# Optimization experiments

Hardware: AMD Instinct MI355X
Metric: run time of the kernel (lower is better)

## Reference

```python
import jax, jax.numpy as jnp
import numpy as np

N_NODES = 50000
N_EDGES = 800000
IN_C = 16
HID_C = 16
OUT_C = 10
N_GRAPHS = 500
EDGE_DIM = 3
MLP_HID = 25
BN_EPS = 1e-5


def setup_inputs() -> dict:
    key = jax.random.key(0)
    ks = iter(jax.random.split(key, 40))

    def nrm(shape, scale=1.0):
        return jax.random.normal(next(ks), shape, dtype=jnp.float32) * scale

    inp = {}
    inp["x"] = nrm((N_NODES, IN_C))
    inp["edge_index"] = jax.random.randint(next(ks), (2, N_EDGES), 0, N_NODES, dtype=jnp.int32)
    inp["edge_attr"] = jax.random.uniform(next(ks), (N_EDGES, EDGE_DIM), dtype=jnp.float32)
    inp["batch"] = jnp.sort(jax.random.randint(next(ks), (N_NODES,), 0, N_GRAPHS, dtype=jnp.int32))

    def bn_params():
        g = jax.random.uniform(next(ks), (MLP_HID,), minval=0.8, maxval=1.2, dtype=jnp.float32)
        b = nrm((MLP_HID,), 0.1)
        mu = nrm((MLP_HID,), 0.1)
        var = jax.random.uniform(next(ks), (MLP_HID,), minval=0.5, maxval=1.5, dtype=jnp.float32)
        return g, b, mu, var

    # edge MLP 1: 3 -> 25 -> IN_C*HID_C
    inp["W1a"] = nrm((EDGE_DIM, MLP_HID), 0.3)
    inp["b1a"] = nrm((MLP_HID,), 0.05)
    inp["g1"], inp["bt1"], inp["m1"], inp["v1"] = bn_params()
    inp["W1b"] = nrm((MLP_HID, IN_C * HID_C), 0.1)
    inp["b1b"] = nrm((IN_C * HID_C,), 0.05)
    inp["root1"] = nrm((IN_C, HID_C), 0.2)
    inp["bias1"] = nrm((HID_C,), 0.05)

    # edge MLP 2: 3 -> 25 -> HID_C*HID_C
    inp["W2a"] = nrm((EDGE_DIM, MLP_HID), 0.3)
    inp["b2a"] = nrm((MLP_HID,), 0.05)
    inp["g2"], inp["bt2"], inp["m2"], inp["v2"] = bn_params()
    inp["W2b"] = nrm((MLP_HID, HID_C * HID_C), 0.1)
    inp["b2b"] = nrm((HID_C * HID_C,), 0.05)
    inp["root2"] = nrm((HID_C, HID_C), 0.2)
    inp["bias2"] = nrm((HID_C,), 0.05)

    # final MLP([HID_C, OUT_C]) -> single plain linear (plain_last)
    inp["fcW"] = nrm((HID_C, OUT_C), 0.2)
    inp["fcb"] = nrm((OUT_C,), 0.05)
    return inp


def _edge_mlp(e, Wa, ba, g, bt, mu, var, Wb, bb):
    # Linear -> BatchNorm(eval) -> ReLU -> (dropout=eval identity) -> Linear
    h = e @ Wa + ba
    h = g * (h - mu) * jax.lax.rsqrt(var + BN_EPS) + bt
    h = jax.nn.relu(h)
    return h @ Wb + bb


def _nnconv(x, src, dst, w_edge, root, bias, out_dim):
    # message: x_j [E,in] times per-edge weight [E,in,out]
    msg = jnp.einsum("ei,eio->eo", x[src], w_edge)
    agg = jax.ops.segment_sum(msg, dst, num_segments=N_NODES)
    deg = jax.ops.segment_sum(jnp.ones((src.shape[0],), msg.dtype), dst, num_segments=N_NODES)
    agg = agg / jnp.maximum(deg, 1.0)[:, None]  # mean aggregation
    return agg + x @ root + bias


def reference(x, edge_index, edge_attr, batch,
              W1a, b1a, g1, bt1, m1, v1, W1b, b1b, root1, bias1,
              W2a, b2a, g2, bt2, m2, v2, W2b, b2b, root2, bias2,
              fcW, fcb):
    src, dst = edge_index[0], edge_index[1]

    w1 = _edge_mlp(edge_attr, W1a, b1a, g1, bt1, m1, v1, W1b, b1b).reshape(-1, IN_C, HID_C)
    x = jax.nn.elu(_nnconv(x, src, dst, w1, root1, bias1, HID_C))

    w2 = _edge_mlp(edge_attr, W2a, b2a, g2, bt2, m2, v2, W2b, b2b).reshape(-1, HID_C, HID_C)
    x = jax.nn.elu(_nnconv(x, src, dst, w2, root2, bias2, HID_C))

    # global mean pooling over graphs
    pooled = jax.ops.segment_sum(x, batch, num_segments=N_GRAPHS)
    cnt = jax.ops.segment_sum(jnp.ones((x.shape[0],), x.dtype), batch, num_segments=N_GRAPHS)
    pooled = pooled / jnp.maximum(cnt, 1.0)[:, None]

    return pooled @ fcW + fcb  # [N_GRAPHS, OUT_C]
```

## Files before the change

kernel.cpp:

```cpp
#include <hip/hip_runtime.h>
#include <math.h>

#define N_NODES 50000
#define N_EDGES 800000
#define IN_C 16
#define HID_C 16
#define OUT_C 10
#define N_GRAPHS 500
#define EDGE_DIM 3
#define MLP_HID 25
#define BN_EPS 1e-5f

#define SCAN_NB ((N_NODES + 255) / 256)

typedef __attribute__((ext_vector_type(8))) _Float16 half8;
typedef __attribute__((ext_vector_type(2))) _Float16 half2v;
typedef __attribute__((ext_vector_type(4))) float f32x4;
union U4H8 { uint4 u; half8 h; half2v p[4]; };
union HU { _Float16 h; unsigned short u; };
union H2U2 { half2v p[2]; uint2 u; };


__global__ __launch_bounds__(256) void setup_kernel(
    const float* __restrict__ W1a, const float* __restrict__ b1a,
    const float* __restrict__ g1, const float* __restrict__ bt1,
    const float* __restrict__ m1, const float* __restrict__ v1,
    const float* __restrict__ W2a, const float* __restrict__ b2a,
    const float* __restrict__ g2, const float* __restrict__ bt2,
    const float* __restrict__ m2, const float* __restrict__ v2,
    const float* __restrict__ W1b, const float* __restrict__ b1b,
    const float* __restrict__ W2b, const float* __restrict__ b2b,
    const int* __restrict__ batch,
    float* __restrict__ AC1, float* __restrict__ AC2,
    unsigned int* __restrict__ WF1, unsigned int* __restrict__ WF2,
    int* __restrict__ goff, int* __restrict__ cnt, int* __restrict__ flag)
{
    const int blk = blockIdx.x;
    const int tid = threadIdx.x;
    if (blk < 7) {
        int t = blk * 256 + tid;
        if (t >= 1664) return;
        const float *Wb, *bb; unsigned int *WH;
        int tl = t;
        if (t < 832) { Wb = W1b; bb = b1b; WH = WF1; }
        else { tl = t - 832; Wb = W2b; bb = b2b; WH = WF2; }
        int m = tl >> 6;
        int L = tl & 63;
        int q = L >> 4, o = L & 15;
        unsigned int hi[8];
        for (int j = 0; j < 8; ++j) {
            int kp = m*32 + q*8 + j;
            int k = kp >> 4, i = kp & 15;
            float w = (k < 25) ? Wb[k*256 + i*16 + o] : bb[i*16 + o];
            HU cv; cv.h = (_Float16)w;
            hi[j] = cv.u;
        }
        int base = (m*64 + L) * 4;
        for (int d = 0; d < 4; ++d)
            WH[base + d] = hi[2*d] | (hi[2*d+1] << 16);
        return;
    }
    if (blk == 7 || blk == 8) {
        if (blk == 7) {
            if (tid < 26) {
                int k = tid;
                if (k < 25) {
                    float sc = g1[k] / sqrtf(v1[k] + BN_EPS);
                    AC1[k*4+0] = sc * W1a[0*MLP_HID+k];
                    AC1[k*4+1] = sc * W1a[1*MLP_HID+k];
                    AC1[k*4+2] = sc * W1a[2*MLP_HID+k];
                    AC1[k*4+3] = sc * (b1a[k] - m1[k]) + bt1[k];
                } else {
                    AC1[100] = 0.f; AC1[101] = 0.f; AC1[102] = 0.f; AC1[103] = 1.f;
                }
            } else if (tid >= 32 && tid < 58) {
                int k = tid - 32;
                if (k < 25) {
                    float sc = g2[k] / sqrtf(v2[k] + BN_EPS);
                    AC2[k*4+0] = sc * W2a[0*MLP_HID+k];
                    AC2[k*4+1] = sc * W2a[1*MLP_HID+k];
                    AC2[k*4+2] = sc * W2a[2*MLP_HID+k];
                    AC2[k*4+3] = sc * (b2a[k] - m2[k]) + bt2[k];
                } else {
                    AC2[100] = 0.f; AC2[101] = 0.f; AC2[102] = 0.f; AC2[103] = 1.f;
                }
            }
        }
        int g = (blk - 7) * 256 + tid;
        if (g <= N_GRAPHS) {
            int lo = 0, hi = N_NODES;
            while (lo < hi) {
                int mid = (lo + hi) >> 1;
                if (batch[mid] < g) lo = mid + 1; else hi = mid;
            }
            goff[g] = lo;
        }
        return;
    }
    int idx = (blk - 9) * 256 + tid;
    if (idx < N_NODES) cnt[idx] = 0;
    if (blk == 9 && tid < SCAN_NB) flag[tid] = 0;
}


__global__ __launch_bounds__(256) void rank_kernel(const int* __restrict__ dst,
                                                   int* __restrict__ cnt,
                                                   int* __restrict__ rank) {
    int e = blockIdx.x * blockDim.x + threadIdx.x;
    if (e < N_EDGES) rank[e] = atomicAdd(&cnt[dst[e]], 1);
}

__global__ __launch_bounds__(256) void scan_single(const int* __restrict__ cnt,
                                                   int* __restrict__ off,
                                                   int* __restrict__ agg,
                                                   int* __restrict__ pre,
                                                   int* __restrict__ flag) {
    __shared__ int lds[256];
    __shared__ int sExc;
    const int b = blockIdx.x, t = threadIdx.x;
    const int idx = b * 256 + t;
    const int v = (idx < N_NODES) ? cnt[idx] : 0;
    lds[t] = v;
    __syncthreads();
    for (int d = 1; d < 256; d <<= 1) {
        int u = (t >= d) ? lds[t - d] : 0;
        __syncthreads();
        lds[t] += u;
        __syncthreads();
    }
    const int total = lds[255];
    if (t == 0) {
        int exc = 0;
        if (b == 0) {
            atomicExch(&pre[0], total);
            __threadfence();
            atomicExch(&flag[0], 2);
        } else {
            atomicExch(&agg[b], total);
            __threadfence();
            atomicExch(&flag[b], 1);
            int j = b - 1;
            while (true) {
                int f;
                do { f = atomicAdd(&flag[j], 0); } while (f == 0);
                if (f == 2) { exc += atomicAdd(&pre[j], 0); break; }
                exc += atomicAdd(&agg[j], 0);
                --j;
            }
            atomicExch(&pre[b], exc + total);
            __threadfence();
            atomicExch(&flag[b], 2);
        }
        sExc = exc;
    }
    __syncthreads();
    const int exc = sExc;
    if (idx < N_NODES) off[idx] = exc + lds[t] - v;
    if (b == SCAN_NB - 1 && t == 255) off[N_NODES] = exc + total;
}


__global__ __launch_bounds__(256) void edge_mfma6_kernel(
    const float* __restrict__ xin,
    const int* __restrict__ src,
    const int* __restrict__ dst,
    const int* __restrict__ rank,
    const int* __restrict__ off,
    const float* __restrict__ eattr,
    const float* __restrict__ AC,
    const unsigned int* __restrict__ WF,
    _Float16* __restrict__ msg_buf)
{
    __shared__ uint4 wf_s[832];
    const int tid = threadIdx.x;
    #pragma unroll
    for (int it = 0; it < 4; ++it) {
        int gi = tid + it*256;
        if (gi < 832) wf_s[gi] = ((const uint4*)WF)[gi];
    }
    __syncthreads();

    const int wave = tid >> 6;
    const int lane = tid & 63;
    const int q    = lane >> 4;
    const int el   = lane & 15;
    const int i0   = (q & 1) * 8;
    const bool bsel = (q >> 1) != 0;
    const int E0   = (blockIdx.x * 4 + wave) * 64;

    const int sAll = src[E0 + lane];
    const int dAll = dst[E0 + lane];
    const int rAll = rank[E0 + lane];
    const int pAll = off[dAll] + rAll;

    int   sT[4];
    float a0[4], a1[4], a2[4];
    #pragma unroll
    for (int t = 0; t < 4; ++t) {
        sT[t] = __shfl(sAll, t*16 + el);
        int e = E0 + t*16 + el;
        a0[t] = eattr[(size_t)e*3+0];
        a1[t] = eattr[(size_t)e*3+1];
        a2[t] = eattr[(size_t)e*3+2];
    }

    U4H8 xf[4];
    #pragma unroll
    for (int t = 0; t < 4; ++t) {
        const float4* xp = (const float4*)(xin + (size_t)sT[t]*16 + i0);
        const float4 xl = xp[0], xh = xp[1];
        const float x8[8] = {xl.x,xl.y,xl.z,xl.w,xh.x,xh.y,xh.z,xh.w};
        #pragma unroll
        for (int j = 0; j < 4; ++j) {
            half2v tv; tv.x = (_Float16)x8[2*j]; tv.y = (_Float16)x8[2*j+1];
            xf[t].p[j] = tv;
        }
    }

    f32x4 acc0 = {0.f,0.f,0.f,0.f}, acc1 = {0.f,0.f,0.f,0.f};
    f32x4 acc2 = {0.f,0.f,0.f,0.f}, acc3 = {0.f,0.f,0.f,0.f};
    #pragma unroll 1
    for (int m = 0; m < 13; ++m) {
        const float4 Ae = *(const float4*)(AC + m*8);
        const float4 Ao = *(const float4*)(AC + m*8 + 4);
        const float A0 = bsel ? Ao.x : Ae.x;
        const float A1 = bsel ? Ao.y : Ae.y;
        const float A2 = bsel ? Ao.z : Ae.z;
        const float A3 = bsel ? Ao.w : Ae.w;
        U4H8 w; w.u = wf_s[m*64 + lane];
        #pragma unroll
        for (int t = 0; t < 4; ++t) {
            float h = fmaxf(fmaf(a2[t], A2, fmaf(a1[t], A1,
                              fmaf(a0[t], A0, A3))), 0.f);
            _Float16 hh = (_Float16)h;
            half2v h2; h2.x = hh; h2.y = hh;
            U4H8 f;
            #pragma unroll
            for (int j = 0; j < 4; ++j) f.p[j] = h2 * xf[t].p[j];
            f32x4 a = (t==0) ? acc0 : (t==1) ? acc1 : (t==2) ? acc2 : acc3;
            a = __builtin_amdgcn_mfma_f32_16x16x32_f16(w.h, f.h, a, 0, 0, 0);
            if (t==0) acc0 = a; else if (t==1) acc1 = a;
            else if (t==2) acc2 = a; else acc3 = a;
        }
    }

    #pragma unroll
    for (int t = 0; t < 4; ++t) {
        int row = __shfl(pAll, t*16 + el);
        f32x4 a = (t==0) ? acc0 : (t==1) ? acc1 : (t==2) ? acc2 : acc3;
        H2U2 cv;
        half2v c01; c01.x = (_Float16)a[0]; c01.y = (_Float16)a[1];
        half2v c23; c23.x = (_Float16)a[2]; c23.y = (_Float16)a[3];
        cv.p[0] = c01; cv.p[1] = c23;
        *(uint2*)(msg_buf + (size_t)row * HID_C + q*4) = cv.u;
    }
}

__global__ __launch_bounds__(256) void node_gather_kernel(
    const float* __restrict__ xin, const _Float16* __restrict__ msg_buf,
    const int* __restrict__ off,
    const float* __restrict__ root, const float* __restrict__ bias,
    float* __restrict__ xout)
{
    int t = blockIdx.x * blockDim.x + threadIdx.x;
    int n = t >> 2;
    int quad = t & 3;
    if (n >= N_NODES) return;
    int lo = off[n], hi = off[n+1];
    float inv = 1.f / fmaxf((float)(hi - lo), 1.f);

    f32x4 s0 = {0.f,0.f,0.f,0.f}, s1 = {0.f,0.f,0.f,0.f};
    int r = lo;
    for (; r + 2 <= hi; r += 2) {
        H2U2 c0; c0.u = *(const uint2*)(msg_buf + (size_t)r     * HID_C + quad*4);
        H2U2 c1; c1.u = *(const uint2*)(msg_buf + (size_t)(r+1) * HID_C + quad*4);
        s0[0] += (float)c0.p[0].x; s0[1] += (float)c0.p[0].y;
        s0[2] += (float)c0.p[1].x; s0[3] += (float)c0.p[1].y;
        s1[0] += (float)c1.p[0].x; s1[1] += (float)c1.p[0].y;
        s1[2] += (float)c1.p[1].x; s1[3] += (float)c1.p[1].y;
    }
    if (r < hi) {
        H2U2 c0; c0.u = *(const uint2*)(msg_buf + (size_t)r * HID_C + quad*4);
        s0[0] += (float)c0.p[0].x; s0[1] += (float)c0.p[0].y;
        s0[2] += (float)c0.p[1].x; s0[3] += (float)c0.p[1].y;
    }

    const float4 bi = *(const float4*)(bias + quad*4);
    float acc0 = fmaf(s0[0] + s1[0], inv, bi.x);
    float acc1 = fmaf(s0[1] + s1[1], inv, bi.y);
    float acc2 = fmaf(s0[2] + s1[2], inv, bi.z);
    float acc3 = fmaf(s0[3] + s1[3], inv, bi.w);

    const float4* xp = (const float4*)(xin + (size_t)n * IN_C);
    const float4 x0 = xp[0], x1 = xp[1], x2 = xp[2], x3 = xp[3];
    const float xr[16] = {x0.x,x0.y,x0.z,x0.w, x1.x,x1.y,x1.z,x1.w,
                          x2.x,x2.y,x2.z,x2.w, x3.x,x3.y,x3.z,x3.w};
    #pragma unroll
    for (int i = 0; i < IN_C; ++i) {
        const float4 rr = *(const float4*)(root + i*HID_C + quad*4);
        acc0 = fmaf(xr[i], rr.x, acc0);
        acc1 = fmaf(xr[i], rr.y, acc1);
        acc2 = fmaf(xr[i], rr.z, acc2);
        acc3 = fmaf(xr[i], rr.w, acc3);
    }
    float4 ov;
    ov.x = acc0 > 0.f ? acc0 : (expf(acc0) - 1.f);
    ov.y = acc1 > 0.f ? acc1 : (expf(acc1) - 1.f);
    ov.z = acc2 > 0.f ? acc2 : (expf(acc2) - 1.f);
    ov.w = acc3 > 0.f ? acc3 : (expf(acc3) - 1.f);
    *(float4*)(xout + (size_t)n*HID_C + quad*4) = ov;
}

__global__ __launch_bounds__(64) void pool_final_kernel(
    const float* __restrict__ xin, const int* __restrict__ goff,
    const float* __restrict__ fcW, const float* __restrict__ fcb,
    float* __restrict__ out)
{
    __shared__ float part[4][HID_C];
    __shared__ float pooled[HID_C];
    int g = blockIdx.x;
    int t = threadIdx.x;
    int c = t & 15, sub = t >> 4;
    int lo = goff[g], hi = goff[g+1];
    float s = 0.f;
    for (int n = lo + sub; n < hi; n += 4)
        s += xin[(size_t)n*HID_C + c];
    part[sub][c] = s;
    __syncthreads();
    if (t < HID_C) {
        pooled[t] = (part[0][t] + part[1][t] + part[2][t] + part[3][t])
                    / fmaxf((float)(hi - lo), 1.f);
    }
    __syncthreads();
    if (t < OUT_C) {
        float acc = fcb[t];
        #pragma unroll
        for (int i = 0; i < HID_C; ++i)
            acc = fmaf(pooled[i], fcW[i*OUT_C+t], acc);
        out[g*OUT_C + t] = acc;
    }
}


extern "C" void kernel_launch(void* const* d_in, const int* in_sizes, int n_in,
                              void* d_out, int out_size, void* d_ws, size_t ws_size,
                              hipStream_t stream)
{
    const float* x     = (const float*)d_in[0];
    const int*   ei    = (const int*)d_in[1];
    const float* eattr = (const float*)d_in[2];
    const int*   batch = (const int*)d_in[3];
    const float* W1a   = (const float*)d_in[4];
    const float* b1a   = (const float*)d_in[5];
    const float* g1    = (const float*)d_in[6];
    const float* bt1   = (const float*)d_in[7];
    const float* m1    = (const float*)d_in[8];
    const float* v1    = (const float*)d_in[9];
    const float* W1b   = (const float*)d_in[10];
    const float* b1b   = (const float*)d_in[11];
    const float* root1 = (const float*)d_in[12];
    const float* bias1 = (const float*)d_in[13];
    const float* W2a   = (const float*)d_in[14];
    const float* b2a   = (const float*)d_in[15];
    const float* g2    = (const float*)d_in[16];
    const float* bt2   = (const float*)d_in[17];
    const float* m2    = (const float*)d_in[18];
    const float* v2    = (const float*)d_in[19];
    const float* W2b   = (const float*)d_in[20];
    const float* b2b   = (const float*)d_in[21];
    const float* root2 = (const float*)d_in[22];
    const float* bias2 = (const float*)d_in[23];
    const float* fcW   = (const float*)d_in[24];
    const float* fcb   = (const float*)d_in[25];

    const int* src = ei;
    const int* dst = ei + N_EDGES;

    float* ws   = (float*)d_ws;
    _Float16* MSG = (_Float16*)ws;
    float* X1   = ws + 12800000;
    float* X2   = ws + 13600000;
    int*   RANK = (int*)(ws + 14400000);
    int*   CNT  = (int*)(ws + 15200000);
    int*   OFF  = (int*)(ws + 15250000);
    int*   GOFF = (int*)(ws + 15300064);
    unsigned int* WF1 = (unsigned int*)(ws + 15300576);
    unsigned int* WF2 = (unsigned int*)(ws + 15303904);
    float* AC1  = ws + 15307232;
    float* AC2  = ws + 15307344;
    int*   AGG  = (int*)(ws + 15307456);
    int*   PRE  = (int*)(ws + 15307712);
    int*   FLAG = (int*)(ws + 15307968);

    setup_kernel<<<9 + SCAN_NB, 256, 0, stream>>>(
        W1a, b1a, g1, bt1, m1, v1, W2a, b2a, g2, bt2, m2, v2,
        W1b, b1b, W2b, b2b, batch, AC1, AC2, WF1, WF2, GOFF, CNT, FLAG);
    rank_kernel<<<N_EDGES/256, 256, 0, stream>>>(dst, CNT, RANK);
    scan_single<<<SCAN_NB, 256, 0, stream>>>(CNT, OFF, AGG, PRE, FLAG);

    edge_mfma6_kernel<<<N_EDGES/256, 256, 0, stream>>>(x, src, dst, RANK, OFF,
                                                       eattr, AC1, WF1, MSG);
    node_gather_kernel<<<(N_NODES*4+255)/256, 256, 0, stream>>>(x, MSG, OFF,
                                                                root1, bias1, X1);

    edge_mfma6_kernel<<<N_EDGES/256, 256, 0, stream>>>(X1, src, dst, RANK, OFF,
                                                       eattr, AC2, WF2, MSG);
    node_gather_kernel<<<(N_NODES*4+255)/256, 256, 0, stream>>>(X1, MSG, OFF,
                                                                root2, bias2, X2);

    pool_final_kernel<<<N_GRAPHS, 64, 0, stream>>>(X2, GOFF, fcW, fcb, (float*)d_out);
}
```

Before: 261.4 us.

## Fuse all stages into a persistent megakernel with software grid barriers

Replaces the eight separate launches (setup, rank, scan, two edge MFMA passes, two gathers, pooling) with one persistent kernel of 1024 blocks. Stages are separated by an atomic generation-counter grid barrier, and the edge and rank phases use grid-stride loops. The aim is to remove per-launch overhead and the idle tails between dependent kernels. In exchange it adds seven global barrier round-trips, relies on all 1024 blocks being co-resident, and caps registers through launch bounds, which could reduce edge-phase occupancy or deadlock if the blocks do not all fit.

```diff
diff --git a/kernel.cpp b/kernel.cpp
--- a/kernel.cpp
+++ b/kernel.cpp
@@ -11,6 +11,8 @@
 #define MLP_HID 25
 #define BN_EPS 1e-5f
 
+#define NB_GRID 1024
+#define N_CHUNKS (N_EDGES / 256)
 #define SCAN_NB ((N_NODES + 255) / 256)
 
 typedef __attribute__((ext_vector_type(8))) _Float16 half8;
@@ -20,47 +22,228 @@
 union HU { _Float16 h; unsigned short u; };
 union H2U2 { half2v p[2]; uint2 u; };
 
-
-__global__ __launch_bounds__(256) void setup_kernel(
+__device__ __forceinline__ void grid_sync(int* bar, int* gen) {
+    __syncthreads();
+    if (threadIdx.x == 0) {
+        __threadfence();
+        int g = atomicAdd(gen, 0);
+        if (atomicAdd(bar, 1) == NB_GRID - 1) {
+            atomicExch(bar, 0);
+            __threadfence();
+            atomicAdd(gen, 1);
+        } else {
+            while (atomicAdd(gen, 0) == g) __builtin_amdgcn_s_sleep(8);
+        }
+        __threadfence();
+    }
+    __syncthreads();
+}
+
+__device__ __forceinline__ void edge_phase(
+    const float* __restrict__ xin, const int* __restrict__ src,
+    const int* __restrict__ dst, const int* __restrict__ rank,
+    const int* __restrict__ off, const float* __restrict__ eattr,
+    const float* __restrict__ AC, const uint4* __restrict__ WF,
+    _Float16* __restrict__ msg_buf, uint4* wf_s)
+{
+    const int tid = threadIdx.x;
+    #pragma unroll
+    for (int it = 0; it < 4; ++it) {
+        int gi = tid + it*256;
+        if (gi < 832) wf_s[gi] = WF[gi];
+    }
+    __syncthreads();
+
+    const int wave = tid >> 6;
+    const int lane = tid & 63;
+    const int q    = lane >> 4;
+    const int el   = lane & 15;
+    const int i0   = (q & 1) * 8;
+    const bool bsel = (q >> 1) != 0;
+
+    for (int chunk = blockIdx.x; chunk < N_CHUNKS; chunk += NB_GRID) {
+        const int E0 = (chunk * 4 + wave) * 64;
+
+        const int sAll = src[E0 + lane];
+        const int dAll = dst[E0 + lane];
+        const int rAll = rank[E0 + lane];
+        const int pAll = off[dAll] + rAll;
+
+        int   sT[4];
+        float a0[4], a1[4], a2[4];
+        #pragma unroll
+        for (int t = 0; t < 4; ++t) {
+            sT[t] = __shfl(sAll, t*16 + el);
+            int e = E0 + t*16 + el;
+            a0[t] = eattr[(size_t)e*3+0];
+            a1[t] = eattr[(size_t)e*3+1];
+            a2[t] = eattr[(size_t)e*3+2];
+        }
+
+        U4H8 xf[4];
+        #pragma unroll
+        for (int t = 0; t < 4; ++t) {
+            const float4* xp = (const float4*)(xin + (size_t)sT[t]*16 + i0);
+            const float4 xl = xp[0], xh = xp[1];
+            const float x8[8] = {xl.x,xl.y,xl.z,xl.w,xh.x,xh.y,xh.z,xh.w};
+            #pragma unroll
+            for (int j = 0; j < 4; ++j) {
+                half2v tv; tv.x = (_Float16)x8[2*j]; tv.y = (_Float16)x8[2*j+1];
+                xf[t].p[j] = tv;
+            }
+        }
+
+        f32x4 acc0 = {0.f,0.f,0.f,0.f}, acc1 = {0.f,0.f,0.f,0.f};
+        f32x4 acc2 = {0.f,0.f,0.f,0.f}, acc3 = {0.f,0.f,0.f,0.f};
+        #pragma unroll 1
+        for (int m = 0; m < 13; ++m) {
+            const float4 Ae = *(const float4*)(AC + m*8);
+            const float4 Ao = *(const float4*)(AC + m*8 + 4);
+            const float A0 = bsel ? Ao.x : Ae.x;
+            const float A1 = bsel ? Ao.y : Ae.y;
+            const float A2 = bsel ? Ao.z : Ae.z;
+            const float A3 = bsel ? Ao.w : Ae.w;
+            U4H8 w; w.u = wf_s[m*64 + lane];
+            #pragma unroll
+            for (int t = 0; t < 4; ++t) {
+                float h = fmaxf(fmaf(a2[t], A2, fmaf(a1[t], A1,
+                                  fmaf(a0[t], A0, A3))), 0.f);
+                _Float16 hh = (_Float16)h;
+                half2v h2; h2.x = hh; h2.y = hh;
+                U4H8 f;
+                #pragma unroll
+                for (int j = 0; j < 4; ++j) f.p[j] = h2 * xf[t].p[j];
+                f32x4 a = (t==0) ? acc0 : (t==1) ? acc1 : (t==2) ? acc2 : acc3;
+                a = __builtin_amdgcn_mfma_f32_16x16x32_f16(w.h, f.h, a, 0, 0, 0);
+                if (t==0) acc0 = a; else if (t==1) acc1 = a;
+                else if (t==2) acc2 = a; else acc3 = a;
+            }
+        }
+
+        #pragma unroll
+        for (int t = 0; t < 4; ++t) {
+            int row = __shfl(pAll, t*16 + el);
+            f32x4 a = (t==0) ? acc0 : (t==1) ? acc1 : (t==2) ? acc2 : acc3;
+            H2U2 cv;
+            half2v c01; c01.x = (_Float16)a[0]; c01.y = (_Float16)a[1];
+            half2v c23; c23.x = (_Float16)a[2]; c23.y = (_Float16)a[3];
+            cv.p[0] = c01; cv.p[1] = c23;
+            *(uint2*)(msg_buf + (size_t)row * HID_C + q*4) = cv.u;
+        }
+    }
+}
+
+__device__ __forceinline__ void gather_phase(
+    const float* __restrict__ xin, const _Float16* __restrict__ msg_buf,
+    const int* __restrict__ off, const float* __restrict__ root,
+    const float* __restrict__ bias, float* __restrict__ xout)
+{
+    int gid = blockIdx.x * 256 + threadIdx.x;
+    int n = gid >> 2;
+    int quad = gid & 3;
+    if (n >= N_NODES) return;
+    int lo = off[n], hi = off[n+1];
+    float inv = 1.f / fmaxf((float)(hi - lo), 1.f);
+
+    f32x4 s0 = {0.f,0.f,0.f,0.f}, s1 = {0.f,0.f,0.f,0.f};
+    int r = lo;
+    for (; r + 2 <= hi; r += 2) {
+        H2U2 c0; c0.u = *(const uint2*)(msg_buf + (size_t)r     * HID_C + quad*4);
+        H2U2 c1; c1.u = *(const uint2*)(msg_buf + (size_t)(r+1) * HID_C + quad*4);
+        s0[0] += (float)c0.p[0].x; s0[1] += (float)c0.p[0].y;
+        s0[2] += (float)c0.p[1].x; s0[3] += (float)c0.p[1].y;
+        s1[0] += (float)c1.p[0].x; s1[1] += (float)c1.p[0].y;
+        s1[2] += (float)c1.p[1].x; s1[3] += (float)c1.p[1].y;
+    }
+    if (r < hi) {
+        H2U2 c0; c0.u = *(const uint2*)(msg_buf + (size_t)r * HID_C + quad*4);
+        s0[0] += (float)c0.p[0].x; s0[1] += (float)c0.p[0].y;
+        s0[2] += (float)c0.p[1].x; s0[3] += (float)c0.p[1].y;
+    }
+
+    const float4 bi = *(const float4*)(bias + quad*4);
+    float acc0 = fmaf(s0[0] + s1[0], inv, bi.x);
+    float acc1 = fmaf(s0[1] + s1[1], inv, bi.y);
+    float acc2 = fmaf(s0[2] + s1[2], inv, bi.z);
+    float acc3 = fmaf(s0[3] + s1[3], inv, bi.w);
+
+    const float4* xp = (const float4*)(xin + (size_t)n * IN_C);
+    const float4 x0 = xp[0], x1 = xp[1], x2 = xp[2], x3 = xp[3];
+    const float xr[16] = {x0.x,x0.y,x0.z,x0.w, x1.x,x1.y,x1.z,x1.w,
+                          x2.x,x2.y,x2.z,x2.w, x3.x,x3.y,x3.z,x3.w};
+    #pragma unroll
+    for (int i = 0; i < IN_C; ++i) {
+        const float4 rr = *(const float4*)(root + i*HID_C + quad*4);
+        acc0 = fmaf(xr[i], rr.x, acc0);
+        acc1 = fmaf(xr[i], rr.y, acc1);
+        acc2 = fmaf(xr[i], rr.z, acc2);
+        acc3 = fmaf(xr[i], rr.w, acc3);
+    }
+    float4 ov;
+    ov.x = acc0 > 0.f ? acc0 : (expf(acc0) - 1.f);
+    ov.y = acc1 > 0.f ? acc1 : (expf(acc1) - 1.f);
+    ov.z = acc2 > 0.f ? acc2 : (expf(acc2) - 1.f);
+    ov.w = acc3 > 0.f ? acc3 : (expf(acc3) - 1.f);
+    *(float4*)(xout + (size_t)n*HID_C + quad*4) = ov;
+}
+
+__global__ __launch_bounds__(256, 4) void mega_kernel(
+    const float* __restrict__ x, const int* __restrict__ ei,
+    const float* __restrict__ eattr, const int* __restrict__ batch,
     const float* __restrict__ W1a, const float* __restrict__ b1a,
     const float* __restrict__ g1, const float* __restrict__ bt1,
     const float* __restrict__ m1, const float* __restrict__ v1,
+    const float* __restrict__ W1b, const float* __restrict__ b1b,
+    const float* __restrict__ root1, const float* __restrict__ bias1,
     const float* __restrict__ W2a, const float* __restrict__ b2a,
     const float* __restrict__ g2, const float* __restrict__ bt2,
     const float* __restrict__ m2, const float* __restrict__ v2,
-    const float* __restrict__ W1b, const float* __restrict__ b1b,
     const float* __restrict__ W2b, const float* __restrict__ b2b,
-    const int* __restrict__ batch,
+    const float* __restrict__ root2, const float* __restrict__ bias2,
+    const float* __restrict__ fcW, const float* __restrict__ fcb,
+    _Float16* __restrict__ MSG, float* __restrict__ X1, float* __restrict__ X2,
+    int* __restrict__ RANK, int* __restrict__ CNT, int* __restrict__ OFF,
+    int* __restrict__ GOFF,
+    unsigned int* __restrict__ WF1, unsigned int* __restrict__ WF2,
     float* __restrict__ AC1, float* __restrict__ AC2,
-    unsigned int* __restrict__ WF1, unsigned int* __restrict__ WF2,
-    int* __restrict__ goff, int* __restrict__ cnt, int* __restrict__ flag)
+    int* __restrict__ AGG, int* __restrict__ PRE, int* __restrict__ FLAG,
+    int* __restrict__ BAR, int* __restrict__ GEN,
+    float* __restrict__ out)
 {
+    __shared__ __align__(16) char smem[13312];
+    uint4* wf_s     = (uint4*)smem;
+    int*   scan_lds = (int*)smem;
+    int*   sExc     = (int*)smem + 256;
+    float* pool_s   = (float*)smem;
+
     const int blk = blockIdx.x;
     const int tid = threadIdx.x;
+    const int* src = ei;
+    const int* dst = ei + N_EDGES;
+
     if (blk < 7) {
         int t = blk * 256 + tid;
-        if (t >= 1664) return;
-        const float *Wb, *bb; unsigned int *WH;
-        int tl = t;
-        if (t < 832) { Wb = W1b; bb = b1b; WH = WF1; }
-        else { tl = t - 832; Wb = W2b; bb = b2b; WH = WF2; }
-        int m = tl >> 6;
-        int L = tl & 63;
-        int q = L >> 4, o = L & 15;
-        unsigned int hi[8];
-        for (int j = 0; j < 8; ++j) {
-            int kp = m*32 + q*8 + j;
-            int k = kp >> 4, i = kp & 15;
-            float w = (k < 25) ? Wb[k*256 + i*16 + o] : bb[i*16 + o];
-            HU cv; cv.h = (_Float16)w;
-            hi[j] = cv.u;
-        }
-        int base = (m*64 + L) * 4;
-        for (int d = 0; d < 4; ++d)
-            WH[base + d] = hi[2*d] | (hi[2*d+1] << 16);
-        return;
-    }
-    if (blk == 7 || blk == 8) {
+        if (t < 1664) {
+            const float *Wb, *bb; unsigned int *WH;
+            int tl = t;
+            if (t < 832) { Wb = W1b; bb = b1b; WH = WF1; }
+            else { tl = t - 832; Wb = W2b; bb = b2b; WH = WF2; }
+            int m = tl >> 6;
+            int L = tl & 63;
+            int q = L >> 4, o = L & 15;
+            unsigned int hi[8];
+            for (int j = 0; j < 8; ++j) {
+                int kp = m*32 + q*8 + j;
+                int k = kp >> 4, i = kp & 15;
+                float w = (k < 25) ? Wb[k*256 + i*16 + o] : bb[i*16 + o];
+                HU cv; cv.h = (_Float16)w;
+                hi[j] = cv.u;
+            }
+            int base = (m*64 + L) * 4;
+            for (int d = 0; d < 4; ++d)
+                WH[base + d] = hi[2*d] | (hi[2*d+1] << 16);
+        }
+    } else if (blk == 7 || blk == 8) {
         if (blk == 7) {
             if (tid < 26) {
                 int k = tid;
@@ -93,251 +276,93 @@
                 int mid = (lo + hi) >> 1;
                 if (batch[mid] < g) lo = mid + 1; else hi = mid;
             }
-            goff[g] = lo;
-        }
-        return;
-    }
-    int idx = (blk - 9) * 256 + tid;
-    if (idx < N_NODES) cnt[idx] = 0;
-    if (blk == 9 && tid < SCAN_NB) flag[tid] = 0;
-}
-
-
-__global__ __launch_bounds__(256) void rank_kernel(const int* __restrict__ dst,
-                                                   int* __restrict__ cnt,
-                                                   int* __restrict__ rank) {
-    int e = blockIdx.x * blockDim.x + threadIdx.x;
-    if (e < N_EDGES) rank[e] = atomicAdd(&cnt[dst[e]], 1);
-}
-
-__global__ __launch_bounds__(256) void scan_single(const int* __restrict__ cnt,
-                                                   int* __restrict__ off,
-                                                   int* __restrict__ agg,
-                                                   int* __restrict__ pre,
-                                                   int* __restrict__ flag) {
-    __shared__ int lds[256];
-    __shared__ int sExc;
-    const int b = blockIdx.x, t = threadIdx.x;
-    const int idx = b * 256 + t;
-    const int v = (idx < N_NODES) ? cnt[idx] : 0;
-    lds[t] = v;
-    __syncthreads();
-    for (int d = 1; d < 256; d <<= 1) {
-        int u = (t >= d) ? lds[t - d] : 0;
+            GOFF[g] = lo;
+        }
+    } else if (blk >= 9 && blk < 9 + SCAN_NB) {
+        int idx = (blk - 9) * 256 + tid;
+        if (idx < N_NODES) CNT[idx] = 0;
+        if (blk == 9 && tid < SCAN_NB) FLAG[tid] = 0;
+    }
+    grid_sync(BAR, GEN);
+
+    for (int e = blk*256 + tid; e < N_EDGES; e += NB_GRID*256)
+        RANK[e] = atomicAdd(&CNT[dst[e]], 1);
+    grid_sync(BAR, GEN);
+
+    if (blk < SCAN_NB) {
+        const int idx = blk*256 + tid;
+        const int v = (idx < N_NODES) ? CNT[idx] : 0;
+        scan_lds[tid] = v;
         __syncthreads();
-        lds[t] += u;
+        for (int d = 1; d < 256; d <<= 1) {
+            int u = (tid >= d) ? scan_lds[tid - d] : 0;
+            __syncthreads();
+            scan_lds[tid] += u;
+            __syncthreads();
+        }
+        const int total = scan_lds[255];
+        if (tid == 0) {
+            int exc = 0;
+            if (blk == 0) {
+                atomicExch(&PRE[0], total);
+                __threadfence();
+                atomicExch(&FLAG[0], 2);
+            } else {
+                atomicExch(&AGG[blk], total);
+                __threadfence();
+                atomicExch(&FLAG[blk], 1);
+                int j = blk - 1;
+                while (true) {
+                    int f;
+                    do { f = atomicAdd(&FLAG[j], 0); } while (f == 0);
+                    if (f == 2) { exc += atomicAdd(&PRE[j], 0); break; }
+                    exc += atomicAdd(&AGG[j], 0);
+                    --j;
+                }
+                atomicExch(&PRE[blk], exc + total);
+                __threadfence();
+                atomicExch(&FLAG[blk], 2);
+            }
+            sExc[0] = exc;
+        }
         __syncthreads();
-    }
-    const int total = lds[255];
-    if (t == 0) {
-        int exc = 0;
-        if (b == 0) {
-            atomicExch(&pre[0], total);
-            __threadfence();
-            atomicExch(&flag[0], 2);
-        } else {
-            atomicExch(&agg[b], total);
-            __threadfence();
-            atomicExch(&flag[b], 1);
-            int j = b - 1;
-            while (true) {
-                int f;
-                do { f = atomicAdd(&flag[j], 0); } while (f == 0);
-                if (f == 2) { exc += atomicAdd(&pre[j], 0); break; }
-                exc += atomicAdd(&agg[j], 0);
-                --j;
-            }
-            atomicExch(&pre[b], exc + total);
-            __threadfence();
-            atomicExch(&flag[b], 2);
-        }
-        sExc = exc;
-    }
-    __syncthreads();
-    const int exc = sExc;
-    if (idx < N_NODES) off[idx] = exc + lds[t] - v;
-    if (b == SCAN_NB - 1 && t == 255) off[N_NODES] = exc + total;
-}
-
-
-__global__ __launch_bounds__(256) void edge_mfma6_kernel(
-    const float* __restrict__ xin,
-    const int* __restrict__ src,
-    const int* __restrict__ dst,
-    const int* __restrict__ rank,
-    const int* __restrict__ off,
-    const float* __restrict__ eattr,
-    const float* __restrict__ AC,
-    const unsigned int* __restrict__ WF,
-    _Float16* __restrict__ msg_buf)
-{
-    __shared__ uint4 wf_s[832];
-    const int tid = threadIdx.x;
-    #pragma unroll
-    for (int it = 0; it < 4; ++it) {
-        int gi = tid + it*256;
-        if (gi < 832) wf_s[gi] = ((const uint4*)WF)[gi];
-    }
-    __syncthreads();
-
-    const int wave = tid >> 6;
-    const int lane = tid & 63;
-    const int q    = lane >> 4;
-    const int el   = lane & 15;
-    const int i0   = (q & 1) * 8;
-    const bool bsel = (q >> 1) != 0;
-    const int E0   = (blockIdx.x * 4 + wave) * 64;
-
-    const int sAll = src[E0 + lane];
-    const int dAll = dst[E0 + lane];
-    const int rAll = rank[E0 + lane];
-    const int pAll = off[dAll] + rAll;
-
-    int   sT[4];
-    float a0[4], a1[4], a2[4];
-    #pragma unroll
-    for (int t = 0; t < 4; ++t) {
-        sT[t] = __shfl(sAll, t*16 + el);
-        int e = E0 + t*16 + el;
-        a0[t] = eattr[(size_t)e*3+0];
-        a1[t] = eattr[(size_t)e*3+1];
-        a2[t] = eattr[(size_t)e*3+2];
-    }
-
-    U4H8 xf[4];
-    #pragma unroll
-    for (int t = 0; t < 4; ++t) {
-        const float4* xp = (const float4*)(xin + (size_t)sT[t]*16 + i0);
-        const float4 xl = xp[0], xh = xp[1];
-        const float x8[8] = {xl.x,xl.y,xl.z,xl.w,xh.x,xh.y,xh.z,xh.w};
-        #pragma unroll
-        for (int j = 0; j < 4; ++j) {
-            half2v tv; tv.x = (_Float16)x8[2*j]; tv.y = (_Float16)x8[2*j+1];
-            xf[t].p[j] = tv;
-        }
-    }
-
-    f32x4 acc0 = {0.f,0.f,0.f,0.f}, acc1 = {0.f,0.f,0.f,0.f};
-    f32x4 acc2 = {0.f,0.f,0.f,0.f}, acc3 = {0.f,0.f,0.f,0.f};
-    #pragma unroll 1
-    for (int m = 0; m < 13; ++m) {
-        const float4 Ae = *(const float4*)(AC + m*8);
-        const float4 Ao = *(const float4*)(AC + m*8 + 4);
-        const float A0 = bsel ? Ao.x : Ae.x;
-        const float A1 = bsel ? Ao.y : Ae.y;
-        const float A2 = bsel ? Ao.z : Ae.z;
-        const float A3 = bsel ? Ao.w : Ae.w;
-        U4H8 w; w.u = wf_s[m*64 + lane];
-        #pragma unroll
-        for (int t = 0; t < 4; ++t) {
-            float h = fmaxf(fmaf(a2[t], A2, fmaf(a1[t], A1,
-                              fmaf(a0[t], A0, A3))), 0.f);
-            _Float16 hh = (_Float16)h;
-            half2v h2; h2.x = hh; h2.y = hh;
-            U4H8 f;
-            #pragma unroll
-            for (int j = 0; j < 4; ++j) f.p[j] = h2 * xf[t].p[j];
-            f32x4 a = (t==0) ? acc0 : (t==1) ? acc1 : (t==2) ? acc2 : acc3;
-            a = __builtin_amdgcn_mfma_f32_16x16x32_f16(w.h, f.h, a, 0, 0, 0);
-            if (t==0) acc0 = a; else if (t==1) acc1 = a;
-            else if (t==2) acc2 = a; else acc3 = a;
-        }
-    }
-
-    #pragma unroll
-    for (int t = 0; t < 4; ++t) {
-        int row = __shfl(pAll, t*16 + el);
-        f32x4 a = (t==0) ? acc0 : (t==1) ? acc1 : (t==2) ? acc2 : acc3;
-        H2U2 cv;
-        half2v c01; c01.x = (_Float16)a[0]; c01.y = (_Float16)a[1];
-        half2v c23; c23.x = (_Float16)a[2]; c23.y = (_Float16)a[3];
-        cv.p[0] = c01; cv.p[1] = c23;
-        *(uint2*)(msg_buf + (size_t)row * HID_C + q*4) = cv.u;
-    }
-}
-
-__global__ __launch_bounds__(256) void node_gather_kernel(
-    const float* __restrict__ xin, const _Float16* __restrict__ msg_buf,
-    const int* __restrict__ off,
-    const float* __restrict__ root, const float* __restrict__ bias,
-    float* __restrict__ xout)
-{
-    int t = blockIdx.x * blockDim.x + threadIdx.x;
-    int n = t >> 2;
-    int quad = t & 3;
-    if (n >= N_NODES) return;
-    int lo = off[n], hi = off[n+1];
-    float inv = 1.f / fmaxf((float)(hi - lo), 1.f);
-
-    f32x4 s0 = {0.f,0.f,0.f,0.f}, s1 = {0.f,0.f,0.f,0.f};
-    int r = lo;
-    for (; r + 2 <= hi; r += 2) {
-        H2U2 c0; c0.u = *(const uint2*)(msg_buf + (size_t)r     * HID_C + quad*4);
-        H2U2 c1; c1.u = *(const uint2*)(msg_buf + (size_t)(r+1) * HID_C + quad*4);
-        s0[0] += (float)c0.p[0].x; s0[1] += (float)c0.p[0].y;
-        s0[2] += (float)c0.p[1].x; s0[3] += (float)c0.p[1].y;
-        s1[0] += (float)c1.p[0].x; s1[1] += (float)c1.p[0].y;
-        s1[2] += (float)c1.p[1].x; s1[3] += (float)c1.p[1].y;
-    }
-    if (r < hi) {
-        H2U2 c0; c0.u = *(const uint2*)(msg_buf + (size_t)r * HID_C + quad*4);
-        s0[0] += (float)c0.p[0].x; s0[1] += (float)c0.p[0].y;
-        s0[2] += (float)c0.p[1].x; s0[3] += (float)c0.p[1].y;
-    }
-
-    const float4 bi = *(const float4*)(bias + quad*4);
-    float acc0 = fmaf(s0[0] + s1[0], inv, bi.x);
-    float acc1 = fmaf(s0[1] + s1[1], inv, bi.y);
-    float acc2 = fmaf(s0[2] + s1[2], inv, bi.z);
-    float acc3 = fmaf(s0[3] + s1[3], inv, bi.w);
-
-    const float4* xp = (const float4*)(xin + (size_t)n * IN_C);
-    const float4 x0 = xp[0], x1 = xp[1], x2 = xp[2], x3 = xp[3];
-    const float xr[16] = {x0.x,x0.y,x0.z,x0.w, x1.x,x1.y,x1.z,x1.w,
-                          x2.x,x2.y,x2.z,x2.w, x3.x,x3.y,x3.z,x3.w};
-    #pragma unroll
-    for (int i = 0; i < IN_C; ++i) {
-        const float4 rr = *(const float4*)(root + i*HID_C + quad*4);
-        acc0 = fmaf(xr[i], rr.x, acc0);
-        acc1 = fmaf(xr[i], rr.y, acc1);
-        acc2 = fmaf(xr[i], rr.z, acc2);
-        acc3 = fmaf(xr[i], rr.w, acc3);
-    }
-    float4 ov;
-    ov.x = acc0 > 0.f ? acc0 : (expf(acc0) - 1.f);
-    ov.y = acc1 > 0.f ? acc1 : (expf(acc1) - 1.f);
-    ov.z = acc2 > 0.f ? acc2 : (expf(acc2) - 1.f);
-    ov.w = acc3 > 0.f ? acc3 : (expf(acc3) - 1.f);
-    *(float4*)(xout + (size_t)n*HID_C + quad*4) = ov;
-}
-
-__global__ __launch_bounds__(64) void pool_final_kernel(
-    const float* __restrict__ xin, const int* __restrict__ goff,
-    const float* __restrict__ fcW, const float* __restrict__ fcb,
-    float* __restrict__ out)
-{
-    __shared__ float part[4][HID_C];
-    __shared__ float pooled[HID_C];
-    int g = blockIdx.x;
-    int t = threadIdx.x;
-    int c = t & 15, sub = t >> 4;
-    int lo = goff[g], hi = goff[g+1];
-    float s = 0.f;
-    for (int n = lo + sub; n < hi; n += 4)
-        s += xin[(size_t)n*HID_C + c];
-    part[sub][c] = s;
-    __syncthreads();
-    if (t < HID_C) {
-        pooled[t] = (part[0][t] + part[1][t] + part[2][t] + part[3][t])
-                    / fmaxf((float)(hi - lo), 1.f);
-    }
-    __syncthreads();
-    if (t < OUT_C) {
-        float acc = fcb[t];
-        #pragma unroll
-        for (int i = 0; i < HID_C; ++i)
-            acc = fmaf(pooled[i], fcW[i*OUT_C+t], acc);
-        out[g*OUT_C + t] = acc;
+        const int exc = sExc[0];
+        if (idx < N_NODES) OFF[idx] = exc + scan_lds[tid] - v;
+        if (blk == SCAN_NB - 1 && tid == 255) OFF[N_NODES] = exc + total;
+    }
+    grid_sync(BAR, GEN);
+
+    edge_phase(x, src, dst, RANK, OFF, eattr, AC1, (const uint4*)WF1, MSG, wf_s);
+    grid_sync(BAR, GEN);
+    gather_phase(x, MSG, OFF, root1, bias1, X1);
+    grid_sync(BAR, GEN);
+    edge_phase(X1, src, dst, RANK, OFF, eattr, AC2, (const uint4*)WF2, MSG, wf_s);
+    grid_sync(BAR, GEN);
+    gather_phase(X1, MSG, OFF, root2, bias2, X2);
+    grid_sync(BAR, GEN);
+
+    if (blk < (N_GRAPHS + 3) / 4) {
+        const int w   = tid >> 6;
+        const int t64 = tid & 63;
+        const int g   = blk * 4 + w;
+        if (g < N_GRAPHS) {
+            const int c = t64 & 15, sub = t64 >> 4;
+            const int lo = GOFF[g], hi = GOFF[g+1];
+            float s = 0.f;
+            for (int n = lo + sub; n < hi; n += 4)
+                s += X2[(size_t)n*HID_C + c];
+            s += __shfl_down(s, 32);
+            s += __shfl_down(s, 16);
+            if (t64 < 16)
+                pool_s[w*16 + t64] = s / fmaxf((float)(hi - lo), 1.f);
+            if (t64 < OUT_C) {
+                float acc = fcb[t64];
+                #pragma unroll
+                for (int i = 0; i < HID_C; ++i)
+                    acc = fmaf(pool_s[w*16 + i], fcW[i*OUT_C+t64], acc);
+                out[g*OUT_C + t64] = acc;
+            }
+        }
     }
 }
 
@@ -373,9 +398,6 @@
     const float* fcW   = (const float*)d_in[24];
     const float* fcb   = (const float*)d_in[25];
 
-    const int* src = ei;
-    const int* dst = ei + N_EDGES;
-
     float* ws   = (float*)d_ws;
     _Float16* MSG = (_Float16*)ws;
     float* X1   = ws + 12800000;
@@ -391,22 +413,14 @@
     int*   AGG  = (int*)(ws + 15307456);
     int*   PRE  = (int*)(ws + 15307712);
     int*   FLAG = (int*)(ws + 15307968);
-
-    setup_kernel<<<9 + SCAN_NB, 256, 0, stream>>>(
-        W1a, b1a, g1, bt1, m1, v1, W2a, b2a, g2, bt2, m2, v2,
-        W1b, b1b, W2b, b2b, batch, AC1, AC2, WF1, WF2, GOFF, CNT, FLAG);
-    rank_kernel<<<N_EDGES/256, 256, 0, stream>>>(dst, CNT, RANK);
-    scan_single<<<SCAN_NB, 256, 0, stream>>>(CNT, OFF, AGG, PRE, FLAG);
-
-    edge_mfma6_kernel<<<N_EDGES/256, 256, 0, stream>>>(x, src, dst, RANK, OFF,
-                                                       eattr, AC1, WF1, MSG);
-    node_gather_kernel<<<(N_NODES*4+255)/256, 256, 0, stream>>>(x, MSG, OFF,
-                                                                root1, bias1, X1);
-
-    edge_mfma6_kernel<<<N_EDGES/256, 256, 0, stream>>>(X1, src, dst, RANK, OFF,
-                                                       eattr, AC2, WF2, MSG);
-    node_gather_kernel<<<(N_NODES*4+255)/256, 256, 0, stream>>>(X1, MSG, OFF,
-                                                                root2, bias2, X2);
-
-    pool_final_kernel<<<N_GRAPHS, 64, 0, stream>>>(X2, GOFF, fcW, fcb, (float*)d_out);
+    int*   BARGEN = (int*)(ws + 15308224);
+
+    hipMemsetAsync(BARGEN, 0, 2 * sizeof(int), stream);
+    mega_kernel<<<NB_GRID, 256, 0, stream>>>(
+        x, ei, eattr, batch,
+        W1a, b1a, g1, bt1, m1, v1, W1b, b1b, root1, bias1,
+        W2a, b2a, g2, bt2, m2, v2, W2b, b2b, root2, bias2,
+        fcW, fcb,
+        MSG, X1, X2, RANK, CNT, OFF, GOFF, WF1, WF2, AC1, AC2,
+        AGG, PRE, FLAG, BARGEN, BARGEN + 1, (float*)d_out);
 }
```

After: 1.009 ms. +286.2%, slower.
